# Performance work log

Measured on AMD Instinct MI355X. Metric: run time of the kernel, lower is better.

## Reference

```python
import jax, jax.numpy as jnp
import numpy as np

B, H, E, IN, OUT = 4096, 1, 8, 256, 256

# BinActive: forward sign(x), backward straight-through clipped to |x|<=1
@jax.custom_vjp
def bin_active(x):
    return jnp.sign(x)

def _ba_fwd(x):
    return jnp.sign(x), x

def _ba_bwd(x, g):
    return (g * (jnp.abs(x) <= 1.0).astype(g.dtype),)

bin_active.defvjp(_ba_fwd, _ba_bwd)

# BinarySoftActivation_Head: hard-threshold gate at 0.5, identity STE backward
@jax.custom_vjp
def bin_gate(x):
    return (x > 0.5).astype(x.dtype)

def _bg_fwd(x):
    return (x > 0.5).astype(x.dtype), None

def _bg_bwd(_, g):
    return (g,)

bin_gate.defvjp(_bg_fwd, _bg_bwd)


def setup_inputs() -> dict:
    key = jax.random.key(0)
    k1, k2, k3, k4, k5 = jax.random.split(key, 5)
    x = jax.random.normal(k1, (B, H, IN), dtype=jnp.float32)
    weight = jax.random.normal(k2, (H, E, IN, OUT), dtype=jnp.float32) * 0.05
    proj_w = jax.random.normal(k3, (E, IN), dtype=jnp.float32) * 0.05  # nn.Linear weight [out,in]
    proj_b = jax.random.normal(k4, (E,), dtype=jnp.float32) * 0.05
    scale = jax.random.normal(k5, (H, 1, OUT), dtype=jnp.float32) * 0.1
    return {"x": x, "weight": weight, "proj_w": proj_w, "proj_b": proj_b, "scale": scale}


def reference(x, weight, proj_w, proj_b, scale):
    # x: [B, H, in]; weight: [H, E, in, out]; proj_w: [E, in]; proj_b: [E]; scale: [H, 1, out]
    xh = jnp.transpose(x, (1, 0, 2))                              # [H, B, in]
    gate = jax.nn.sigmoid(jnp.einsum('hbi,ei->hbe', xh, proj_w) + proj_b)
    gate = bin_gate(gate)                                         # hard 0/1 gates [H, B, E]
    # per-sample synthesized weight (the huge intermediate): [H, B, in, out]
    w = jnp.einsum('hbe,heio->hbio', gate, weight)
    xb = bin_active(xh)                                           # sign-binarized activations
    wb = bin_active(w)                                            # sign-binarized weights
    y = jnp.einsum('hbi,hbio->hbo', xb, wb)                       # batched GEMV, [H, B, out]
    y = y * scale                                                 # per-head learned scale
    return jnp.transpose(y, (1, 0, 2))                            # [B, H, out]
```

## Files before the change

kernel.cpp:

```cpp
#include <hip/hip_runtime.h>
#include <stdint.h>

#define B_N   4096
#define E_N   8
#define IN_N  256
#define OUT_N 256
#define NMASK 256

__global__ __launch_bounds__(256) void build_wbits(const float* __restrict__ W,
                                                   uint64_t* __restrict__ wbits) {
    const int lane = threadIdx.x & 63;
    const int wv   = threadIdx.x >> 6;
    const int o    = blockIdx.x * 4 + wv;
    const int j    = blockIdx.y;
    const int i    = j * 64 + lane;

    float w[E_N];
    #pragma unroll
    for (int e = 0; e < E_N; ++e)
        w[e] = W[((size_t)e * IN_N + i) * OUT_N + o];

    float slo[16];
    slo[0] = 0.0f;
    #pragma unroll
    for (int m = 1; m < 16; ++m) {
        const int hb = 31 - __builtin_clz(m);
        slo[m] = slo[m ^ (1 << hb)] + w[hb];
    }

    #pragma unroll 1
    for (int lo = 0; lo < 16; ++lo) {
        float t[16];
        t[0] = slo[lo];
        #pragma unroll
        for (int h = 1; h < 16; ++h) {
            const int hb = 31 - __builtin_clz(h);
            t[h] = t[h ^ (1 << hb)] + w[4 + hb];
        }
        #pragma unroll
        for (int h = 0; h < 16; ++h) {
            const int mask = h * 16 + lo;
            const unsigned long long bits = __ballot(t[h] < 0.0f);
            if (lane == 0)
                wbits[((size_t)mask * OUT_N + o) * 4 + j] = bits;
        }
    }
}

__global__ __launch_bounds__(256) void gate_gemv(const float* __restrict__ x,
                                                 const float* __restrict__ pw,
                                                 const float* __restrict__ pb,
                                                 const float* __restrict__ scale,
                                                 const uint64_t* __restrict__ wbits,
                                                 float* __restrict__ out) {
    const int lane = threadIdx.x & 63;
    const int wv   = threadIdx.x >> 6;
    const int b    = blockIdx.x * 4 + wv;

    const float* xb = x + (size_t)b * IN_N;
    float xs[4];
    #pragma unroll
    for (int j = 0; j < 4; ++j) xs[j] = xb[j * 64 + lane];

    uint64_t xw[4], zw[4];
    #pragma unroll
    for (int j = 0; j < 4; ++j) {
        xw[j] = __ballot(xs[j] <  0.0f);
        zw[j] = __ballot(xs[j] == 0.0f);
    }

    uint32_t mask = 0u;
    #pragma unroll
    for (int e = 0; e < E_N; ++e) {
        const float* pwe = pw + e * IN_N;
        float v = xs[0] * pwe[lane];
        v += xs[1] * pwe[ 64 + lane];
        v += xs[2] * pwe[128 + lane];
        v += xs[3] * pwe[192 + lane];
        v += __shfl_xor(v, 1);  v += __shfl_xor(v, 2);  v += __shfl_xor(v, 4);
        v += __shfl_xor(v, 8);  v += __shfl_xor(v, 16); v += __shfl_xor(v, 32);
        if (v + pb[e] > 0.0f) mask |= (1u << e);
    }

    float* ob = out + (size_t)b * OUT_N;
    if (mask != 0u) {
        const uint64_t* wp = wbits + (size_t)mask * (OUT_N * 4);
        const int nz = __popcll(zw[0]) + __popcll(zw[1]) +
                       __popcll(zw[2]) + __popcll(zw[3]);
        const int base = IN_N - nz;
        #pragma unroll
        for (int q = 0; q < 4; ++q) {
            const int o = q * 64 + lane;
            const uint64_t* w4 = wp + (size_t)o * 4;
            const ulonglong2 a  = *reinterpret_cast<const ulonglong2*>(w4);
            const ulonglong2 c  = *reinterpret_cast<const ulonglong2*>(w4 + 2);
            const int d = __popcll((xw[0] ^ a.x) & ~zw[0])
                        + __popcll((xw[1] ^ a.y) & ~zw[1])
                        + __popcll((xw[2] ^ c.x) & ~zw[2])
                        + __popcll((xw[3] ^ c.y) & ~zw[3]);
            ob[o] = (float)(base - 2 * d) * scale[o];
        }
    } else {
        #pragma unroll
        for (int q = 0; q < 4; ++q) ob[q * 64 + lane] = 0.0f;
    }
}

extern "C" void kernel_launch(void* const* d_in, const int* in_sizes, int n_in,
                              void* d_out, int out_size, void* d_ws, size_t ws_size,
                              hipStream_t stream) {
    const float* x     = (const float*)d_in[0];
    const float* W     = (const float*)d_in[1];
    const float* pw    = (const float*)d_in[2];
    const float* pb    = (const float*)d_in[3];
    const float* scale = (const float*)d_in[4];
    float*       out   = (float*)d_out;

    uint64_t* wbits = (uint64_t*)d_ws;

    hipLaunchKernelGGL(build_wbits, dim3(OUT_N / 4, 4), dim3(256), 0, stream,
                       W, wbits);
    hipLaunchKernelGGL(gate_gemv, dim3(B_N / 4), dim3(256), 0, stream,
                       x, pw, pb, scale, wbits, out);
}
```

Before: 82.23 us.

## Move gating and x-binarization into the table-build kernel to run concurrently

The per-sample gate projection and sign/zero bitmask extraction move from the GEMV kernel into the first kernel, which gains extra blocks that run alongside the weight-bit table build. The second kernel then only reads the precomputed bitmasks and gate mask and does the popcount GEMV. The aim is to hide the gate computation under the table build and shorten the critical path of the second kernel. The cost is an extra round-trip of the bitmasks and masks through global workspace memory.

```diff
diff --git a/kernel.cpp b/kernel.cpp
--- a/kernel.cpp
+++ b/kernel.cpp
@@ -7,97 +7,121 @@
 #define OUT_N 256
 #define NMASK 256
 
-__global__ __launch_bounds__(256) void build_wbits(const float* __restrict__ W,
-                                                   uint64_t* __restrict__ wbits) {
+#define WBITS_U64   (NMASK * OUT_N * 4)
+#define XZ_OFF_U64  WBITS_U64
+
+__global__ __launch_bounds__(256) void prep(const float* __restrict__ W,
+                                            const float* __restrict__ x,
+                                            const float* __restrict__ pw,
+                                            const float* __restrict__ pb,
+                                            uint64_t* __restrict__ wbits,
+                                            uint64_t* __restrict__ xz,
+                                            uint32_t* __restrict__ masks) {
     const int lane = threadIdx.x & 63;
     const int wv   = threadIdx.x >> 6;
-    const int o    = blockIdx.x * 4 + wv;
-    const int j    = blockIdx.y;
-    const int i    = j * 64 + lane;
 
-    float w[E_N];
-    #pragma unroll
-    for (int e = 0; e < E_N; ++e)
-        w[e] = W[((size_t)e * IN_N + i) * OUT_N + o];
+    if (blockIdx.x < 256) {
+        const int ox = blockIdx.x & 63;
+        const int j  = blockIdx.x >> 6;
+        const int o  = ox * 4 + wv;
+        const int i  = j * 64 + lane;
 
-    float slo[16];
-    slo[0] = 0.0f;
-    #pragma unroll
-    for (int m = 1; m < 16; ++m) {
-        const int hb = 31 - __builtin_clz(m);
-        slo[m] = slo[m ^ (1 << hb)] + w[hb];
-    }
+        float w[E_N];
+        #pragma unroll
+        for (int e = 0; e < E_N; ++e)
+            w[e] = W[((size_t)e * IN_N + i) * OUT_N + o];
 
-    #pragma unroll 1
-    for (int lo = 0; lo < 16; ++lo) {
-        float t[16];
-        t[0] = slo[lo];
+        float slo[16];
+        slo[0] = 0.0f;
         #pragma unroll
-        for (int h = 1; h < 16; ++h) {
-            const int hb = 31 - __builtin_clz(h);
-            t[h] = t[h ^ (1 << hb)] + w[4 + hb];
+        for (int m = 1; m < 16; ++m) {
+            const int hb = 31 - __builtin_clz(m);
+            slo[m] = slo[m ^ (1 << hb)] + w[hb];
         }
+
+        #pragma unroll 1
+        for (int lo = 0; lo < 16; ++lo) {
+            float t[16];
+            t[0] = slo[lo];
+            #pragma unroll
+            for (int h = 1; h < 16; ++h) {
+                const int hb = 31 - __builtin_clz(h);
+                t[h] = t[h ^ (1 << hb)] + w[4 + hb];
+            }
+            #pragma unroll
+            for (int h = 0; h < 16; ++h) {
+                const int mask = h * 16 + lo;
+                const unsigned long long bits = __ballot(t[h] < 0.0f);
+                if (lane == 0)
+                    wbits[((size_t)mask * OUT_N + o) * 4 + j] = bits;
+            }
+        }
+    } else {
+        const int b = (blockIdx.x - 256) * 4 + wv;
+
+        const float* xb = x + (size_t)b * IN_N;
+        float xs[4];
         #pragma unroll
-        for (int h = 0; h < 16; ++h) {
-            const int mask = h * 16 + lo;
-            const unsigned long long bits = __ballot(t[h] < 0.0f);
-            if (lane == 0)
-                wbits[((size_t)mask * OUT_N + o) * 4 + j] = bits;
+        for (int j = 0; j < 4; ++j) xs[j] = xb[j * 64 + lane];
+
+        uint64_t xw[4], zw[4];
+        #pragma unroll
+        for (int j = 0; j < 4; ++j) {
+            xw[j] = __ballot(xs[j] <  0.0f);
+            zw[j] = __ballot(xs[j] == 0.0f);
+        }
+
+        uint32_t mask = 0u;
+        #pragma unroll
+        for (int e = 0; e < E_N; ++e) {
+            const float* pwe = pw + e * IN_N;
+            float v = xs[0] * pwe[lane];
+            v += xs[1] * pwe[ 64 + lane];
+            v += xs[2] * pwe[128 + lane];
+            v += xs[3] * pwe[192 + lane];
+            v += __shfl_xor(v, 1);  v += __shfl_xor(v, 2);  v += __shfl_xor(v, 4);
+            v += __shfl_xor(v, 8);  v += __shfl_xor(v, 16); v += __shfl_xor(v, 32);
+            if (v + pb[e] > 0.0f) mask |= (1u << e);
+        }
+
+        if (lane == 0) {
+            uint64_t* s = xz + (size_t)b * 8;
+            s[0] = xw[0]; s[1] = xw[1]; s[2] = xw[2]; s[3] = xw[3];
+            s[4] = zw[0]; s[5] = zw[1]; s[6] = zw[2]; s[7] = zw[3];
+            masks[b] = mask;
         }
     }
 }
 
-__global__ __launch_bounds__(256) void gate_gemv(const float* __restrict__ x,
-                                                 const float* __restrict__ pw,
-                                                 const float* __restrict__ pb,
+__global__ __launch_bounds__(256) void popc_gemv(const uint64_t* __restrict__ wbits,
+                                                 const uint64_t* __restrict__ xz,
+                                                 const uint32_t* __restrict__ masks,
                                                  const float* __restrict__ scale,
-                                                 const uint64_t* __restrict__ wbits,
                                                  float* __restrict__ out) {
     const int lane = threadIdx.x & 63;
     const int wv   = threadIdx.x >> 6;
     const int b    = blockIdx.x * 4 + wv;
 
-    const float* xb = x + (size_t)b * IN_N;
-    float xs[4];
-    #pragma unroll
-    for (int j = 0; j < 4; ++j) xs[j] = xb[j * 64 + lane];
+    const uint32_t m = masks[b];
+    float* ob = out + (size_t)b * OUT_N;
 
-    uint64_t xw[4], zw[4];
-    #pragma unroll
-    for (int j = 0; j < 4; ++j) {
-        xw[j] = __ballot(xs[j] <  0.0f);
-        zw[j] = __ballot(xs[j] == 0.0f);
-    }
-
-    uint32_t mask = 0u;
-    #pragma unroll
-    for (int e = 0; e < E_N; ++e) {
-        const float* pwe = pw + e * IN_N;
-        float v = xs[0] * pwe[lane];
-        v += xs[1] * pwe[ 64 + lane];
-        v += xs[2] * pwe[128 + lane];
-        v += xs[3] * pwe[192 + lane];
-        v += __shfl_xor(v, 1);  v += __shfl_xor(v, 2);  v += __shfl_xor(v, 4);
-        v += __shfl_xor(v, 8);  v += __shfl_xor(v, 16); v += __shfl_xor(v, 32);
-        if (v + pb[e] > 0.0f) mask |= (1u << e);
-    }
-
-    float* ob = out + (size_t)b * OUT_N;
-    if (mask != 0u) {
-        const uint64_t* wp = wbits + (size_t)mask * (OUT_N * 4);
-        const int nz = __popcll(zw[0]) + __popcll(zw[1]) +
-                       __popcll(zw[2]) + __popcll(zw[3]);
-        const int base = IN_N - nz;
+    if (m != 0u) {
+        const uint64_t* s = xz + (size_t)b * 8;
+        const uint64_t x0 = s[0], x1 = s[1], x2 = s[2], x3 = s[3];
+        const uint64_t z0 = s[4], z1 = s[5], z2 = s[6], z3 = s[7];
+        const int base = IN_N - (__popcll(z0) + __popcll(z1) +
+                                 __popcll(z2) + __popcll(z3));
+        const uint64_t* wp = wbits + (size_t)m * (OUT_N * 4);
         #pragma unroll
         for (int q = 0; q < 4; ++q) {
             const int o = q * 64 + lane;
             const uint64_t* w4 = wp + (size_t)o * 4;
-            const ulonglong2 a  = *reinterpret_cast<const ulonglong2*>(w4);
-            const ulonglong2 c  = *reinterpret_cast<const ulonglong2*>(w4 + 2);
-            const int d = __popcll((xw[0] ^ a.x) & ~zw[0])
-                        + __popcll((xw[1] ^ a.y) & ~zw[1])
-                        + __popcll((xw[2] ^ c.x) & ~zw[2])
-                        + __popcll((xw[3] ^ c.y) & ~zw[3]);
+            const ulonglong2 a = *reinterpret_cast<const ulonglong2*>(w4);
+            const ulonglong2 c = *reinterpret_cast<const ulonglong2*>(w4 + 2);
+            const int d = __popcll((x0 ^ a.x) & ~z0)
+                        + __popcll((x1 ^ a.y) & ~z1)
+                        + __popcll((x2 ^ c.x) & ~z2)
+                        + __popcll((x3 ^ c.y) & ~z3);
             ob[o] = (float)(base - 2 * d) * scale[o];
         }
     } else {
@@ -117,9 +141,11 @@
     float*       out   = (float*)d_out;
 
     uint64_t* wbits = (uint64_t*)d_ws;
+    uint64_t* xz    = (uint64_t*)d_ws + XZ_OFF_U64;
+    uint32_t* masks = (uint32_t*)((uint64_t*)d_ws + XZ_OFF_U64 + (size_t)B_N * 8);
 
-    hipLaunchKernelGGL(build_wbits, dim3(OUT_N / 4, 4), dim3(256), 0, stream,
-                       W, wbits);
-    hipLaunchKernelGGL(gate_gemv, dim3(B_N / 4), dim3(256), 0, stream,
-                       x, pw, pb, scale, wbits, out);
+    hipLaunchKernelGGL(prep, dim3(256 + B_N / 4), dim3(256), 0, stream,
+                       W, x, pw, pb, wbits, xz, masks);
+    hipLaunchKernelGGL(popc_gemv, dim3(B_N / 4), dim3(256), 0, stream,
+                       wbits, xz, masks, scale, out);
 }
```

Result: no change. 81.69 us (-0.7%).
